# Kernel tuning notes

Measured on AMD Instinct MI355X. Metric: run time of the kernel, lower is better.

Reference implementation:

```python
import jax, jax.numpy as jnp
import numpy as np

C = 25          # bands / channels (fixed by module)
HID = 50        # fc hidden dim
EPS = 1e-8


def _dwconv(x, w, pad):
    # x: [B,C,H,W], w: [C,1,kh,kw] depthwise (feature_group_count=C)
    return jax.lax.conv_general_dilated(
        x, w, window_strides=(1, 1), padding=((pad, pad), (pad, pad)),
        dimension_numbers=("NCHW", "OIHW", "NCHW"), feature_group_count=C)


def setup_inputs() -> dict:
    key = jax.random.key(0)
    ks = jax.random.split(key, 8)
    B, H, W = 32, 256, 256
    x = jax.random.normal(ks[0], (B, C, H, W), dtype=jnp.float32)
    w_dw7 = jax.random.normal(ks[1], (C, 1, 7, 7), dtype=jnp.float32) * 0.1
    b_dw7 = jax.random.normal(ks[2], (C,), dtype=jnp.float32) * 0.1
    w_dw3 = jax.random.normal(ks[3], (C, 1, 3, 3), dtype=jnp.float32) * 0.1
    fc1_w = jax.random.normal(ks[4], (HID, C), dtype=jnp.float32) * 0.2
    fc1_b = jax.random.normal(ks[5], (HID,), dtype=jnp.float32) * 0.1
    fc2_w = jax.random.normal(ks[6], (C, HID), dtype=jnp.float32) * 0.2
    fc2_b = jax.random.normal(ks[7], (C,), dtype=jnp.float32) * 0.1
    return {"x": x, "w_dw7": w_dw7, "b_dw7": b_dw7, "w_dw3": w_dw3,
            "fc1_w": fc1_w, "fc1_b": fc1_b, "fc2_w": fc2_w, "fc2_b": fc2_b,
            "bandstype": 0}


def reference(x, w_dw7, b_dw7, w_dw3, fc1_w, fc1_b, fc2_w, fc2_b, bandstype):
    # bandstype==0 -> 'hypertrack_nir' branch
    input_x = x
    h = _dwconv(x, w_dw7, pad=1) + b_dw7[None, :, None, None]   # [B,C,H-4,W-4]
    h = jax.nn.gelu(h, approximate=False)                        # nn.GELU exact
    h = _dwconv(h, w_dw3, pad=1)
    g = jnp.mean(h, axis=(2, 3))                                 # GAP -> [B,C]
    g = jax.nn.relu(g @ fc1_w.T + fc1_b)
    s = jax.nn.sigmoid(g @ fc2_w.T + fc2_b)                      # [B,C]
    gate = (s * s) / (s * s + EPS)
    gated = input_x * gate[:, :, None, None]                     # [B,C,H,W]
    # topk over all 25 channels, gather channels per batch
    _, idx = jax.lax.top_k(s, C)                                 # [B,C] int32
    rank_x = jnp.take_along_axis(gated, idx[:, :, None, None], axis=1)
    x_selected = rank_x[:, :-15, :, :]   # top-10 channels
    x_plug = rank_x[:, 10:, :, :]        # remaining 15
    return (x_selected, x_plug, idx)
```

## Files before the change

### kernel.cpp

```cpp
#include <hip/hip_runtime.h>
#include <math.h>

#define NC 25
#define NHID 50
#define NB 32
#define NH 256
#define NW 256
#define NOH 252
#define NOW 252

#define CHUNK 28
#define NCHUNK 9
#define INROWS 34

template<int NR>
__device__ __forceinline__ void conv_pass(
    const float (*ring)[264], const float* wgt, int lbase, int lane,
    float (*acc)[4])
{
#pragma unroll
    for (int r = 0; r < NR + 6; ++r) {
        const float* rp = &ring[lbase + r][4 * lane];
        float xv[13];
        xv[3] = rp[3];
        const float4 q1 = *(const float4*)(rp + 4);
        const float4 q2 = *(const float4*)(rp + 8);
        xv[4] = q1.x; xv[5] = q1.y; xv[6] = q1.z; xv[7] = q1.w;
        xv[8] = q2.x; xv[9] = q2.y; xv[10] = q2.z; xv[11] = q2.w;
        xv[12] = rp[12];
#pragma unroll
        for (int j = 0; j < NR; ++j) {
            const int ky = r - j;
            if (ky >= 0 && ky < 7) {
#pragma unroll
                for (int cc = 0; cc < 4; ++cc) {
                    float s = 0.f;
#pragma unroll
                    for (int kx = 0; kx < 7; ++kx)
                        s = fmaf(wgt[ky * 7 + kx], xv[cc + kx + 3], s);
                    acc[j][cc] += s;
                }
            }
        }
    }
}

__global__ __launch_bounds__(256) void stats_kernel(
    const float* __restrict__ x, const float* __restrict__ w7,
    const float* __restrict__ b7, float* __restrict__ partial)
{
    const int bid   = blockIdx.x;
    const int plane = bid / NCHUNK;
    const int chunk = bid - plane * NCHUNK;
    const int c     = plane % NC;
    const int r0    = chunk * CHUNK;
    const float* xp = x + (size_t)plane * (NH * NW);

    float wgt[49];
#pragma unroll
    for (int i = 0; i < 49; ++i) wgt[i] = w7[c * 49 + i];
    const float bias = b7[c];

    __shared__ __attribute__((aligned(16))) float ring[INROWS][264];
    __shared__ float red[4][9];

    const int tid  = threadIdx.x;
    const int wave = tid >> 6;
    const int lane = tid & 63;

    for (int idx = tid; idx < INROWS * 66; idx += 256) {
        const int row = idx / 66;
        const int p   = idx - row * 66;
        const int iy  = r0 - 1 + row;
        float4 v = make_float4(0.f, 0.f, 0.f, 0.f);
        if (p >= 1 && p <= 64 && iy >= 0 && iy < NH)
            v = *(const float4*)&xp[iy * NW + 4 * (p - 1)];
        *(float4*)&ring[row][4 * p] = v;
    }
    __syncthreads();

    float tot = 0.f, r0s = 0.f, r251s = 0.f, c0s = 0.f, c251s = 0.f;
    float g00 = 0.f, g0R = 0.f, gR0 = 0.f, gRR = 0.f;

    if (lane < 63) {
        const int oyF0 = r0 + wave * 7;
        const int oyF1 = oyF0 + 4;

        {
            float acc[4][4];
#pragma unroll
            for (int j = 0; j < 4; ++j)
#pragma unroll
                for (int cc = 0; cc < 4; ++cc) acc[j][cc] = 0.f;
            conv_pass<4>(ring, wgt, oyF0 - r0, lane, acc);
#pragma unroll
            for (int j = 0; j < 4; ++j) {
                const int oy = oyF0 + j;
                float g[4];
#pragma unroll
                for (int cc = 0; cc < 4; ++cc) {
                    float h = acc[j][cc] + bias;
                    g[cc] = 0.5f * h * (1.0f + erff(h * 0.70710678f));
                }
                const float s4 = (g[0] + g[1]) + (g[2] + g[3]);
                tot += s4;
                if (lane == 0)  c0s   += g[0];
                if (lane == 62) c251s += g[3];
                if (oy == 0)   { r0s   += s4; if (lane == 0) g00 += g[0]; if (lane == 62) g0R += g[3]; }
                if (oy == 251) { r251s += s4; if (lane == 0) gR0 += g[0]; if (lane == 62) gRR += g[3]; }
            }
        }
        {
            float acc[3][4];
#pragma unroll
            for (int j = 0; j < 3; ++j)
#pragma unroll
                for (int cc = 0; cc < 4; ++cc) acc[j][cc] = 0.f;
            conv_pass<3>(ring, wgt, oyF1 - r0, lane, acc);
#pragma unroll
            for (int j = 0; j < 3; ++j) {
                const int oy = oyF1 + j;
                float g[4];
#pragma unroll
                for (int cc = 0; cc < 4; ++cc) {
                    float h = acc[j][cc] + bias;
                    g[cc] = 0.5f * h * (1.0f + erff(h * 0.70710678f));
                }
                const float s4 = (g[0] + g[1]) + (g[2] + g[3]);
                tot += s4;
                if (lane == 0)  c0s   += g[0];
                if (lane == 62) c251s += g[3];
                if (oy == 0)   { r0s   += s4; if (lane == 0) g00 += g[0]; if (lane == 62) g0R += g[3]; }
                if (oy == 251) { r251s += s4; if (lane == 0) gR0 += g[0]; if (lane == 62) gRR += g[3]; }
            }
        }
    }

    float st[9] = {tot, r0s, r251s, c0s, c251s, g00, g0R, gR0, gRR};
#pragma unroll
    for (int i = 0; i < 9; ++i) {
        float v = st[i];
        for (int off = 32; off > 0; off >>= 1) v += __shfl_down(v, off, 64);
        st[i] = v;
    }
    if (lane == 0) {
#pragma unroll
        for (int i = 0; i < 9; ++i) red[wave][i] = st[i];
    }
    __syncthreads();
    if (tid < 9)
        partial[(size_t)bid * 9 + tid] =
            (red[0][tid] + red[1][tid]) + (red[2][tid] + red[3][tid]);
}

__global__ __launch_bounds__(64) void mlp_kernel(
    const float* __restrict__ partial, const float* __restrict__ w3,
    const float* __restrict__ fc1w, const float* __restrict__ fc1b,
    const float* __restrict__ fc2w, const float* __restrict__ fc2b,
    float* __restrict__ idx_out, float* __restrict__ gate_ws,
    int* __restrict__ src_ws)
{
    const int b = blockIdx.x;
    const int t = threadIdx.x;
    __shared__ float mean_s[NC], hid_s[NHID], s_s[NC];

    if (t < NC) {
        const float* base = partial + (size_t)(b * NC + t) * NCHUNK * 9;
        double acc[9];
#pragma unroll
        for (int i = 0; i < 9; ++i) acc[i] = 0.0;
        for (int ch = 0; ch < NCHUNK; ++ch)
#pragma unroll
            for (int i = 0; i < 9; ++i) acc[i] += (double)base[ch * 9 + i];

        float T = (float)acc[0], R0 = (float)acc[1], R251 = (float)acc[2];
        float C0 = (float)acc[3], C251 = (float)acc[4];
        float g00 = (float)acc[5], g0R = (float)acc[6];
        float gR0 = (float)acc[7], gRR = (float)acc[8];

        float ER[3] = {R251, 0.f, R0};
        float EC[3] = {C251, 0.f, C0};
        float CR[3][3] = {{gRR, 0.f, gR0}, {0.f, 0.f, 0.f}, {g0R, 0.f, g00}};
        float m = 0.f;
#pragma unroll
        for (int ky = 0; ky < 3; ++ky)
#pragma unroll
            for (int kx = 0; kx < 3; ++kx) {
                float S = T - ER[ky] - EC[kx] + CR[ky][kx];
                m += w3[t * 9 + ky * 3 + kx] * S;
            }
        mean_s[t] = m * (1.0f / (252.0f * 252.0f));
    }
    __syncthreads();
    if (t < NHID) {
        float a = fc1b[t];
#pragma unroll
        for (int cc = 0; cc < NC; ++cc) a += mean_s[cc] * fc1w[t * NC + cc];
        hid_s[t] = fmaxf(a, 0.f);
    }
    __syncthreads();
    if (t < NC) {
        float a = fc2b[t];
#pragma unroll
        for (int j = 0; j < NHID; ++j) a += hid_s[j] * fc2w[t * NHID + j];
        s_s[t] = 1.0f / (1.0f + expf(-a));
    }
    __syncthreads();
    if (t < NC) {
        float s = s_s[t];
        int rank = 0;
        for (int c2 = 0; c2 < NC; ++c2) {
            float s2 = s_s[c2];
            if (s2 > s || (s2 == s && c2 < t)) rank++;
        }
        float gate = (s * s) / (s * s + 1e-8f);
        idx_out[b * NC + rank] = (float)t;
        gate_ws[b * NC + rank] = gate;
        src_ws[b * NC + rank]  = t;
    }
}

__global__ __launch_bounds__(256) void gather_kernel(
    const float* __restrict__ x, const float* __restrict__ gate_ws,
    const int* __restrict__ src_ws, float* __restrict__ out)
{
    const int bid = blockIdx.x;
    const int seg = bid & 3;
    const int p   = bid >> 2;
    const int b   = p / NC;
    const int j   = p - b * NC;
    const int src = src_ws[p];
    const float gate = gate_ws[p];

    const float4* xp = (const float4*)(x + ((size_t)(b * NC + src)) * (NH * NW))
                       + seg * 4096;
    float* dst;
    if (j < 10) dst = out + ((size_t)(b * 10 + j)) * (NH * NW);
    else dst = out + (size_t)NB * 10 * (NH * NW) + ((size_t)(b * 15 + (j - 10))) * (NH * NW);
    float4* dp = (float4*)dst + seg * 4096;

    const int t = threadIdx.x;
#pragma unroll 4
    for (int i = t; i < 4096; i += 256) {
        float4 v = xp[i];
        v.x *= gate; v.y *= gate; v.z *= gate; v.w *= gate;
        dp[i] = v;
    }
}

extern "C" void kernel_launch(void* const* d_in, const int* in_sizes, int n_in,
                              void* d_out, int out_size, void* d_ws, size_t ws_size,
                              hipStream_t stream)
{
    const float* x    = (const float*)d_in[0];
    const float* w7   = (const float*)d_in[1];
    const float* b7   = (const float*)d_in[2];
    const float* w3   = (const float*)d_in[3];
    const float* fc1w = (const float*)d_in[4];
    const float* fc1b = (const float*)d_in[5];
    const float* fc2w = (const float*)d_in[6];
    const float* fc2b = (const float*)d_in[7];
    float* out = (float*)d_out;

    float* partial = (float*)d_ws;
    float* gate_ws = partial + NB * NC * NCHUNK * 9;
    int*   src_ws  = (int*)(gate_ws + NB * NC);

    float* idx_out = out + (size_t)NB * 10 * (NH * NW) + (size_t)NB * 15 * (NH * NW);

    stats_kernel<<<NB * NC * NCHUNK, 256, 0, stream>>>(x, w7, b7, partial);
    mlp_kernel<<<NB, 64, 0, stream>>>(partial, w3, fc1w, fc1b, fc2w, fc2b,
                                      idx_out, gate_ws, src_ws);
    gather_kernel<<<NB * NC * 4, 256, 0, stream>>>(x, gate_ws, src_ws, out);
}
```

Before: 520.2 us.

## Merge conv row passes into one 7-row pass and use fast erf GELU

Each wave now computes all 7 output rows in a single sliding pass over 13 ring rows instead of two passes (4 and 3 rows). That cuts redundant shared-memory loads of the overlapping input rows. The library erff is replaced by a rational-polynomial erf approximation using hardware rcp and exp2 to lower transcendental cost. Launch bounds request 4 blocks per CU. The trade-offs are a bigger accumulator register footprint and slightly different rounding in the GELU and the FMA ordering.

After: 713.1 us. 1.37x slower.

```diff
diff --git a/kernel.cpp b/kernel.cpp
--- a/kernel.cpp
+++ b/kernel.cpp
@@ -13,39 +13,55 @@
 #define NCHUNK 9
 #define INROWS 34
 
+__device__ __forceinline__ float gelu_exact(float h)
+{
+    const float x  = h * 0.70710678118654752f;
+    const float ax = fabsf(x);
+    const float t  = __builtin_amdgcn_rcpf(fmaf(0.3275911f, ax, 1.0f));
+    float p = fmaf(1.061405429f, t, -1.453152027f);
+    p = fmaf(p, t, 1.421413741f);
+    p = fmaf(p, t, -0.284496736f);
+    p = fmaf(p, t, 0.254829592f);
+    p = p * t;
+    const float e  = __builtin_amdgcn_exp2f(ax * ax * -1.4426950408889634f);
+    float er = fmaf(-p, e, 1.0f);
+    er = copysignf(er, x);
+    return 0.5f * h * (1.0f + er);
+}
+
 template<int NR>
-__device__ __forceinline__ void conv_pass(
+__device__ __forceinline__ void conv_pass7(
     const float (*ring)[264], const float* wgt, int lbase, int lane,
     float (*acc)[4])
 {
 #pragma unroll
     for (int r = 0; r < NR + 6; ++r) {
         const float* rp = &ring[lbase + r][4 * lane];
-        float xv[13];
-        xv[3] = rp[3];
+        const float4 q0 = *(const float4*)(rp);
         const float4 q1 = *(const float4*)(rp + 4);
         const float4 q2 = *(const float4*)(rp + 8);
-        xv[4] = q1.x; xv[5] = q1.y; xv[6] = q1.z; xv[7] = q1.w;
-        xv[8] = q2.x; xv[9] = q2.y; xv[10] = q2.z; xv[11] = q2.w;
-        xv[12] = rp[12];
+        const float4 q3 = *(const float4*)(rp + 12);
+        float xv[10];
+        xv[0] = q0.w;
+        xv[1] = q1.x; xv[2] = q1.y; xv[3] = q1.z; xv[4] = q1.w;
+        xv[5] = q2.x; xv[6] = q2.y; xv[7] = q2.z; xv[8] = q2.w;
+        xv[9] = q3.x;
 #pragma unroll
         for (int j = 0; j < NR; ++j) {
             const int ky = r - j;
             if (ky >= 0 && ky < 7) {
 #pragma unroll
                 for (int cc = 0; cc < 4; ++cc) {
-                    float s = 0.f;
 #pragma unroll
                     for (int kx = 0; kx < 7; ++kx)
-                        s = fmaf(wgt[ky * 7 + kx], xv[cc + kx + 3], s);
-                    acc[j][cc] += s;
+                        acc[j][cc] = fmaf(wgt[ky * 7 + kx], xv[cc + kx], acc[j][cc]);
                 }
             }
         }
     }
 }
 
-__global__ __launch_bounds__(256) void stats_kernel(
+__global__ __launch_bounds__(256, 4) void stats_kernel(
     const float* __restrict__ x, const float* __restrict__ w7,
     const float* __restrict__ b7, float* __restrict__ partial)
 {
@@ -83,56 +99,27 @@
     float g00 = 0.f, g0R = 0.f, gR0 = 0.f, gRR = 0.f;
 
     if (lane < 63) {
-        const int oyF0 = r0 + wave * 7;
-        const int oyF1 = oyF0 + 4;
-
-        {
-            float acc[4][4];
-#pragma unroll
-            for (int j = 0; j < 4; ++j)
-#pragma unroll
-                for (int cc = 0; cc < 4; ++cc) acc[j][cc] = 0.f;
-            conv_pass<4>(ring, wgt, oyF0 - r0, lane, acc);
-#pragma unroll
-            for (int j = 0; j < 4; ++j) {
-                const int oy = oyF0 + j;
-                float g[4];
-#pragma unroll
-                for (int cc = 0; cc < 4; ++cc) {
-                    float h = acc[j][cc] + bias;
-                    g[cc] = 0.5f * h * (1.0f + erff(h * 0.70710678f));
-                }
-                const float s4 = (g[0] + g[1]) + (g[2] + g[3]);
-                tot += s4;
-                if (lane == 0)  c0s   += g[0];
-                if (lane == 62) c251s += g[3];
-                if (oy == 0)   { r0s   += s4; if (lane == 0) g00 += g[0]; if (lane == 62) g0R += g[3]; }
-                if (oy == 251) { r251s += s4; if (lane == 0) gR0 += g[0]; if (lane == 62) gRR += g[3]; }
-            }
-        }
-        {
-            float acc[3][4];
-#pragma unroll
-            for (int j = 0; j < 3; ++j)
-#pragma unroll
-                for (int cc = 0; cc < 4; ++cc) acc[j][cc] = 0.f;
-            conv_pass<3>(ring, wgt, oyF1 - r0, lane, acc);
-#pragma unroll
-            for (int j = 0; j < 3; ++j) {
-                const int oy = oyF1 + j;
-                float g[4];
-#pragma unroll
-                for (int cc = 0; cc < 4; ++cc) {
-                    float h = acc[j][cc] + bias;
-                    g[cc] = 0.5f * h * (1.0f + erff(h * 0.70710678f));
-                }
-                const float s4 = (g[0] + g[1]) + (g[2] + g[3]);
-                tot += s4;
-                if (lane == 0)  c0s   += g[0];
-                if (lane == 62) c251s += g[3];
-                if (oy == 0)   { r0s   += s4; if (lane == 0) g00 += g[0]; if (lane == 62) g0R += g[3]; }
-                if (oy == 251) { r251s += s4; if (lane == 0) gR0 += g[0]; if (lane == 62) gRR += g[3]; }
-            }
+        float acc[7][4];
+#pragma unroll
+        for (int j = 0; j < 7; ++j)
+#pragma unroll
+            for (int cc = 0; cc < 4; ++cc) acc[j][cc] = 0.f;
+
+        conv_pass7<7>(ring, wgt, wave * 7, lane, acc);
+
+#pragma unroll
+        for (int j = 0; j < 7; ++j) {
+            const int oy = r0 + wave * 7 + j;
+            float g[4];
+#pragma unroll
+            for (int cc = 0; cc < 4; ++cc)
+                g[cc] = gelu_exact(acc[j][cc] + bias);
+            const float s4 = (g[0] + g[1]) + (g[2] + g[3]);
+            tot += s4;
+            if (lane == 0)  c0s   += g[0];
+            if (lane == 62) c251s += g[3];
+            if (oy == 0)   { r0s   += s4; if (lane == 0) g00 += g[0]; if (lane == 62) g0R += g[3]; }
+            if (oy == 251) { r251s += s4; if (lane == 0) gR0 += g[0]; if (lane == 62) gRR += g[3]; }
         }
     }
 
```
